# Kernel tuning notes

Measured on AMD Instinct MI355X. Metric: run time of the kernel, lower is better.

## Reference

```python
import jax, jax.numpy as jnp
import numpy as np

N = 16384          # input points
IN_PLANES = 64
OUT_PLANES = 128
STRIDE = 4
NSAMPLE = 16
M = N // STRIDE    # sampled points
EPS = 1e-5         # BatchNorm eps


def setup_inputs() -> dict:
    key = jax.random.key(0)
    k1, k2, k3 = jax.random.split(key, 3)
    p = jax.random.uniform(k1, (N, 3), dtype=jnp.float32) * 10.0   # xyz coords
    x = jax.random.normal(k2, (N, IN_PLANES), dtype=jnp.float32)
    o = jnp.array([N], dtype=jnp.int32)                            # single-batch offsets
    W = jax.random.normal(k3, (OUT_PLANES, 3 + IN_PLANES), dtype=jnp.float32) / np.sqrt(3 + IN_PLANES)
    gamma = jnp.ones((OUT_PLANES,), dtype=jnp.float32)
    beta = jnp.zeros((OUT_PLANES,), dtype=jnp.float32)
    return {"p": p, "x": x, "o": o, "W": W, "gamma": gamma, "beta": beta}


def _fps(p, m):
    """Furthest point sampling, starting from point 0 (matches pointops)."""
    n = p.shape[0]

    def step(carry, _):
        dist, last = carry
        d = jnp.sum((p - p[last]) ** 2, axis=1)       # (N,)
        dist = jnp.minimum(dist, d)
        nxt = jnp.argmax(dist).astype(jnp.int32)
        return (dist, nxt), nxt

    init = (jnp.full((n,), 1e10, dtype=jnp.float32), jnp.int32(0))
    _, idxs = jax.lax.scan(step, init, None, length=m - 1)
    return jnp.concatenate([jnp.zeros((1,), jnp.int32), idxs])


def _transition_down(p, x, W, gamma, beta):
    idx = _fps(p, M)
    n_p = p[idx]                                                    # (M,3)
    # kNN query: squared distances (M,N), take NSAMPLE nearest
    d2 = (jnp.sum(n_p ** 2, axis=1, keepdims=True)
          + jnp.sum(p ** 2, axis=1)[None, :]
          - 2.0 * n_p @ p.T)
    _, knn = jax.lax.top_k(-d2, NSAMPLE)                            # (M,NSAMPLE)
    rel = p[knn] - n_p[:, None, :]                                  # grouped relative xyz (M,S,3)
    feats = jnp.concatenate([rel, x[knn]], axis=-1)                 # (M,S,3+C) use_xyz=True
    y = jnp.einsum('msc,oc->mso', feats, W)                         # linear, no bias (M,S,O)
    # BatchNorm1d (training mode): normalize over batch (M) and length (S) dims
    mean = jnp.mean(y, axis=(0, 1))
    var = jnp.var(y, axis=(0, 1))
    y = (y - mean) * jax.lax.rsqrt(var + EPS) * gamma + beta
    y = jax.nn.relu(y)
    y = jnp.max(y, axis=1)                                          # MaxPool1d over nsample -> (M,O)
    return n_p, y


def reference(p, x, o, W, gamma, beta):
    n_p, y = _transition_down(p, x, W, gamma, beta)
    n_o = (o // STRIDE).astype(jnp.int32)
    return (n_p, y, n_o)
```

## Files before the change

### kernel.cpp

```cpp
#include <hip/hip_runtime.h>

#define N_PTS   16384
#define M_PTS   4096
#define NS      16
#define C_IN    64
#define C_FEAT  67
#define C_OUT   128
#define QPB     8
#define GEMM_BLOCKS (M_PTS / QPB)
#define N_O_POS (M_PTS*3 + M_PTS*C_OUT)

__global__ __launch_bounds__(1024)
void fps_kernel(const float* __restrict__ p, int* __restrict__ fidx)
{
#pragma clang fp contract(off)
    const int t    = threadIdx.x;
    const int lane = t & 63;
    const int wid  = t >> 6;

    float px[16], py[16], pz[16], dist[16];
#pragma unroll
    for (int k = 0; k < 16; ++k) {
        const int i = t + (k << 10);
        px[k] = p[3*i+0]; py[k] = p[3*i+1]; pz[k] = p[3*i+2];
        dist[k] = 1e10f;
    }

    __shared__ float swv[16];
    __shared__ int   swi[16];
    __shared__ float sq[4];

    if (t == 0) fidx[0] = 0;
    float qx = p[0], qy = p[1], qz = p[2];

    for (int it = 1; it < M_PTS; ++it) {
        float bv = -1.0f; int bi = 0x7fffffff;
#pragma unroll
        for (int k = 0; k < 16; ++k) {
            const float dx = px[k] - qx;
            const float dy = py[k] - qy;
            const float dz = pz[k] - qz;
            float d = dx*dx + dy*dy;
            d = d + dz*dz;
            const float nd = fminf(dist[k], d);
            dist[k] = nd;
            const bool take = nd > bv;
            bv = take ? nd : bv;
            bi = take ? (t + (k << 10)) : bi;
        }
#pragma unroll
        for (int off = 1; off < 64; off <<= 1) {
            const float ov = __shfl_xor(bv, off, 64);
            const int   oi = __shfl_xor(bi, off, 64);
            const bool take = (ov > bv) || (ov == bv && oi < bi);
            bv = take ? ov : bv;  bi = take ? oi : bi;
        }
        if (lane == 0) { swv[wid] = bv; swi[wid] = bi; }
        __syncthreads();
        float v2 = swv[lane & 15]; int i2 = swi[lane & 15];
#pragma unroll
        for (int off = 1; off < 16; off <<= 1) {
            const float ov = __shfl_xor(v2, off, 64);
            const int   oi = __shfl_xor(i2, off, 64);
            const bool take = (ov > v2) || (ov == v2 && oi < i2);
            v2 = take ? ov : v2;  i2 = take ? oi : i2;
        }
        const int cur = i2;
        if (t == (cur & 1023)) {
            const int k = cur >> 10;
            float ax = 0.f, ay = 0.f, az = 0.f;
#pragma unroll
            for (int k2 = 0; k2 < 16; ++k2) {
                if (k2 == k) { ax = px[k2]; ay = py[k2]; az = pz[k2]; }
            }
            sq[0] = ax; sq[1] = ay; sq[2] = az;
            fidx[it] = cur;
        }
        __syncthreads();
        qx = sq[0]; qy = sq[1]; qz = sq[2];
    }
}

__global__ __launch_bounds__(256)
void knn_kernel(const float* __restrict__ p, const int* __restrict__ fidx,
                int* __restrict__ knn_out, float* __restrict__ out_np)
{
    const int lane = threadIdx.x & 63;
    const int wid  = threadIdx.x >> 6;
    const int m    = blockIdx.x * 4 + wid;

    const int iq = fidx[m];
    const float qx = p[3*iq+0], qy = p[3*iq+1], qz = p[3*iq+2];
    if (lane == 0) { out_np[m*3+0] = qx; out_np[m*3+1] = qy; out_np[m*3+2] = qz; }

    float d16[16]; int i16[16];
#pragma unroll
    for (int jj = 0; jj < 16; ++jj) {
        const int j = jj*64 + lane;
        const float dx = p[3*j+0]-qx, dy = p[3*j+1]-qy, dz = p[3*j+2]-qz;
        d16[jj] = fmaf(dx, dx, fmaf(dy, dy, dz*dz));
        i16[jj] = j;
    }
    float wv = d16[0];
#pragma unroll
    for (int k = 1; k < 16; ++k) wv = fmaxf(wv, d16[k]);

    for (int jj = 16; jj < 256; ++jj) {
        const int j = jj*64 + lane;
        const float dx = p[3*j+0]-qx, dy = p[3*j+1]-qy, dz = p[3*j+2]-qz;
        const float d = fmaf(dx, dx, fmaf(dy, dy, dz*dz));
        if (d < wv) {
            bool done = false;
#pragma unroll
            for (int k = 0; k < 16; ++k) {
                const bool is = (!done) && (d16[k] == wv);
                d16[k] = is ? d : d16[k];
                i16[k] = is ? j : i16[k];
                done = done || is;
            }
            wv = d16[0];
#pragma unroll
            for (int k = 1; k < 16; ++k) wv = fmaxf(wv, d16[k]);
        }
    }

    float lmv; int lmi;
    {
        lmv = d16[0]; lmi = i16[0];
#pragma unroll
        for (int k = 1; k < 16; ++k) {
            const bool tk = (d16[k] < lmv) || (d16[k] == lmv && i16[k] < lmi);
            lmv = tk ? d16[k] : lmv;  lmi = tk ? i16[k] : lmi;
        }
    }
    int mykn = 0;
    for (int r = 0; r < 16; ++r) {
        float v = lmv; int ii = lmi;
#pragma unroll
        for (int off = 1; off < 64; off <<= 1) {
            const float ov = __shfl_xor(v, off, 64);
            const int   oi = __shfl_xor(ii, off, 64);
            const bool tk = (ov < v) || (ov == v && oi < ii);
            v = tk ? ov : v;  ii = tk ? oi : ii;
        }
        if (lane == r) mykn = ii;
        if (lmi == ii) {
#pragma unroll
            for (int k = 0; k < 16; ++k)
                d16[k] = (i16[k] == ii) ? 3.4e38f : d16[k];
            lmv = d16[0]; lmi = i16[0];
#pragma unroll
            for (int k = 1; k < 16; ++k) {
                const bool tk = (d16[k] < lmv) || (d16[k] == lmv && i16[k] < lmi);
                lmv = tk ? d16[k] : lmv;  lmi = tk ? i16[k] : lmi;
            }
        }
    }
    if (lane < 16) knn_out[m*16 + lane] = mykn;
}

template <int PHASE>
__global__ __launch_bounds__(256)
void gemm_kernel(const float* __restrict__ p, const float* __restrict__ x,
                 const int* __restrict__ knn, const float* __restrict__ W,
                 const float* __restrict__ np_buf, float* __restrict__ part,
                 const float* __restrict__ scsh, float* __restrict__ out_y)
{
    __shared__ float w_lds[C_OUT * C_FEAT];
    __shared__ float feats[NS * 68];
    __shared__ float tmp[512];

    const int tid = threadIdx.x;
    for (int e = tid; e < C_OUT * C_FEAT; e += 256) w_lds[e] = W[e];
    __syncthreads();

    const int o  = tid & 127;
    const int s0 = (tid >> 7) * 8;
    float wreg[C_FEAT];
#pragma unroll
    for (int c = 0; c < C_FEAT; ++c) wreg[c] = w_lds[o * C_FEAT + c];

    float sc = 0.f, sh = 0.f;
    if (PHASE == 1) { sc = scsh[o]; sh = scsh[128 + o]; }

    float lsum = 0.f, lsq = 0.f;

    for (int ml = 0; ml < QPB; ++ml) {
        const int m = blockIdx.x * QPB + ml;
        __syncthreads();
        for (int e = tid; e < NS * C_FEAT; e += 256) {
            const int s = e / C_FEAT;
            const int c = e - s * C_FEAT;
            const int j = knn[m * NS + s];
            float v;
            if (c < 3) v = p[3*j + c] - np_buf[m*3 + c];
            else       v = x[j * C_IN + (c - 3)];
            feats[s * 68 + c] = v;
        }
        __syncthreads();

        float mx = 0.0f;
#pragma unroll
        for (int s8 = 0; s8 < 8; ++s8) {
            const int s = s0 + s8;
            const float4* fr = (const float4*)&feats[s * 68];
            float a = 0.f;
#pragma unroll
            for (int c4 = 0; c4 < 16; ++c4) {
                const float4 f = fr[c4];
                a = fmaf(f.x, wreg[c4*4+0], a);
                a = fmaf(f.y, wreg[c4*4+1], a);
                a = fmaf(f.z, wreg[c4*4+2], a);
                a = fmaf(f.w, wreg[c4*4+3], a);
            }
            a = fmaf(feats[s*68+64], wreg[64], a);
            a = fmaf(feats[s*68+65], wreg[65], a);
            a = fmaf(feats[s*68+66], wreg[66], a);
            if (PHASE == 0) { lsum += a; lsq = fmaf(a, a, lsq); }
            else {
                float v = fmaf(a, sc, sh);
                v = fmaxf(v, 0.f);
                mx = fmaxf(mx, v);
            }
        }
        if (PHASE == 1) {
            tmp[tid] = mx;
            __syncthreads();
            if (tid < 128) out_y[m * C_OUT + o] = fmaxf(tmp[tid], tmp[tid + 128]);
        }
    }

    if (PHASE == 0) {
        tmp[tid] = lsum; tmp[256 + tid] = lsq;
        __syncthreads();
        if (tid < 128) {
            part[blockIdx.x * 256 + o]       = tmp[tid] + tmp[tid + 128];
            part[blockIdx.x * 256 + 128 + o] = tmp[256 + tid] + tmp[256 + tid + 128];
        }
    }
}

__global__ __launch_bounds__(128)
void stats_kernel(const float* __restrict__ part, const float* __restrict__ gamma,
                  const float* __restrict__ beta, float* __restrict__ scsh,
                  float* __restrict__ out)
{
    const int o = threadIdx.x;
    float s = 0.f, s2 = 0.f;
    for (int b = 0; b < GEMM_BLOCKS; ++b) {
        s  += part[b * 256 + o];
        s2 += part[b * 256 + 128 + o];
    }
    const float inv  = 1.0f / 65536.0f;
    const float mean = s * inv;
    const float var  = fmaf(s2, inv, -mean * mean);
    const float sc   = gamma[o] * rsqrtf(var + 1e-5f);
    const float sh   = fmaf(-mean, sc, beta[o]);
    scsh[o] = sc; scsh[128 + o] = sh;
    if (o == 0) out[N_O_POS] = 4096.0f;
}

extern "C" void kernel_launch(void* const* d_in, const int* in_sizes, int n_in,
                              void* d_out, int out_size, void* d_ws, size_t ws_size,
                              hipStream_t stream)
{
    const float* p     = (const float*)d_in[0];
    const float* x     = (const float*)d_in[1];
    const float* W     = (const float*)d_in[3];
    const float* gamma = (const float*)d_in[4];
    const float* beta  = (const float*)d_in[5];
    float* out = (float*)d_out;

    int*   fidx = (int*)d_ws;
    int*   knn  = fidx + M_PTS;
    float* part = (float*)(knn + M_PTS * NS);
    float* scsh = part + GEMM_BLOCKS * 256;

    float* out_np = out;
    float* out_y  = out + M_PTS * 3;

    fps_kernel<<<dim3(1), dim3(1024), 0, stream>>>(p, fidx);
    knn_kernel<<<dim3(M_PTS / 4), dim3(256), 0, stream>>>(p, fidx, knn, out_np);
    gemm_kernel<0><<<dim3(GEMM_BLOCKS), dim3(256), 0, stream>>>(
        p, x, knn, W, out_np, part, scsh, out_y);
    stats_kernel<<<dim3(1), dim3(128), 0, stream>>>(part, gamma, beta, scsh, out);
    gemm_kernel<1><<<dim3(GEMM_BLOCKS), dim3(256), 0, stream>>>(
        p, x, knn, W, out_np, part, scsh, out_y);
}
```

Before: 10.16 ms.

## Morton-sort points and skip FPS distance updates via per-thread bounding boxes

```diff
diff --git a/kernel.cpp b/kernel.cpp
--- a/kernel.cpp
+++ b/kernel.cpp
@@ -10,74 +10,152 @@
 #define GEMM_BLOCKS (M_PTS / QPB)
 #define N_O_POS (M_PTS*3 + M_PTS*C_OUT)
 
+#define FPS_T   512
+#define PPT     32
+
+__device__ __forceinline__ unsigned spread3(unsigned x)
+{
+    x = (x | (x << 16)) & 0x030000FFu;
+    x = (x | (x << 8))  & 0x0300F00Fu;
+    x = (x | (x << 4))  & 0x030C30C3u;
+    x = (x | (x << 2))  & 0x09249249u;
+    return x;
+}
+
 __global__ __launch_bounds__(1024)
-void fps_kernel(const float* __restrict__ p, int* __restrict__ fidx)
+void morton_sort_kernel(const float* __restrict__ p, unsigned* __restrict__ keys)
+{
+    __shared__ unsigned k_lds[N_PTS];
+    const int t = threadIdx.x;
+#pragma unroll
+    for (int s = 0; s < 16; ++s) {
+        const int i = t + (s << 10);
+        const float xx = p[3*i+0], yy = p[3*i+1], zz = p[3*i+2];
+        unsigned cx = (unsigned)fminf(fmaxf(xx * 6.4f, 0.f), 63.f);
+        unsigned cy = (unsigned)fminf(fmaxf(yy * 6.4f, 0.f), 63.f);
+        unsigned cz = (unsigned)fminf(fmaxf(zz * 6.4f, 0.f), 63.f);
+        const unsigned code = spread3(cx) | (spread3(cy) << 1) | (spread3(cz) << 2);
+        k_lds[i] = (code << 14) | (unsigned)i;
+    }
+    __syncthreads();
+    for (unsigned kk = 2; kk <= (unsigned)N_PTS; kk <<= 1) {
+        for (unsigned jj = kk >> 1; jj >= 1; jj >>= 1) {
+            for (int s = 0; s < 16; ++s) {
+                const int i = t + (s << 10);
+                const int ixj = i ^ (int)jj;
+                if (ixj > i) {
+                    const unsigned a = k_lds[i], b = k_lds[ixj];
+                    const bool up = ((i & kk) == 0);
+                    if (up ? (a > b) : (a < b)) { k_lds[i] = b; k_lds[ixj] = a; }
+                }
+            }
+            __syncthreads();
+        }
+    }
+#pragma unroll
+    for (int s = 0; s < 16; ++s) {
+        const int i = t + (s << 10);
+        keys[i] = k_lds[i];
+    }
+}
+
+__global__ __launch_bounds__(FPS_T)
+void fps_kernel(const float* __restrict__ p, const unsigned* __restrict__ keys,
+                int* __restrict__ fidx)
 {
 #pragma clang fp contract(off)
     const int t    = threadIdx.x;
     const int lane = t & 63;
     const int wid  = t >> 6;
 
-    float px[16], py[16], pz[16], dist[16];
-#pragma unroll
-    for (int k = 0; k < 16; ++k) {
-        const int i = t + (k << 10);
-        px[k] = p[3*i+0]; py[k] = p[3*i+1]; pz[k] = p[3*i+2];
+    float px[PPT], py[PPT], pz[PPT], dist[PPT];
+    int   oi[PPT];
+    float lox =  3e38f, loy =  3e38f, loz =  3e38f;
+    float hix = -3e38f, hiy = -3e38f, hiz = -3e38f;
+
+#pragma unroll
+    for (int k = 0; k < PPT; ++k) {
+        const unsigned key = keys[t * PPT + k];
+        const int j = (int)(key & 16383u);
+        oi[k] = j;
+        px[k] = p[3*j+0]; py[k] = p[3*j+1]; pz[k] = p[3*j+2];
         dist[k] = 1e10f;
-    }
-
-    __shared__ float swv[16];
-    __shared__ int   swi[16];
-    __shared__ float sq[4];
+        lox = fminf(lox, px[k]); hix = fmaxf(hix, px[k]);
+        loy = fminf(loy, py[k]); hiy = fmaxf(hiy, py[k]);
+        loz = fminf(loz, pz[k]); hiz = fmaxf(hiz, pz[k]);
+    }
+
+    __shared__ float  swv[8];
+    __shared__ int    swi[8];
+    __shared__ float4 sqv;
 
     if (t == 0) fidx[0] = 0;
-    float qx = p[0], qy = p[1], qz = p[2];
+#pragma unroll
+    for (int k = 0; k < PPT; ++k)
+        if (oi[k] == 0) sqv = make_float4(px[k], py[k], pz[k], 0.f);
+
+    float mymax = 1e10f;  int myidx = -1;
+    float bx = 0.f, by = 0.f, bz = 0.f;
+    int lastwin = 0;
+
+    __syncthreads();
 
     for (int it = 1; it < M_PTS; ++it) {
-        float bv = -1.0f; int bi = 0x7fffffff;
-#pragma unroll
-        for (int k = 0; k < 16; ++k) {
-            const float dx = px[k] - qx;
-            const float dy = py[k] - qy;
-            const float dz = pz[k] - qz;
-            float d = dx*dx + dy*dy;
-            d = d + dz*dz;
-            const float nd = fminf(dist[k], d);
-            dist[k] = nd;
-            const bool take = nd > bv;
-            bv = take ? nd : bv;
-            bi = take ? (t + (k << 10)) : bi;
-        }
-#pragma unroll
-        for (int off = 1; off < 64; off <<= 1) {
-            const float ov = __shfl_xor(bv, off, 64);
-            const int   oi = __shfl_xor(bi, off, 64);
-            const bool take = (ov > bv) || (ov == bv && oi < bi);
-            bv = take ? ov : bv;  bi = take ? oi : bi;
-        }
-        if (lane == 0) { swv[wid] = bv; swi[wid] = bi; }
-        __syncthreads();
-        float v2 = swv[lane & 15]; int i2 = swi[lane & 15];
-#pragma unroll
-        for (int off = 1; off < 16; off <<= 1) {
+        const float4 q4 = sqv;
+        const float qx = q4.x, qy = q4.y, qz = q4.z;
+
+        const float gx = fmaxf(fmaxf(lox - qx, qx - hix), 0.f);
+        const float gy = fmaxf(fmaxf(loy - qy, qy - hiy), 0.f);
+        const float gz = fmaxf(fmaxf(loz - qz, qz - hiz), 0.f);
+        const float dlow = (gx*gx + gy*gy + gz*gz) * 0.99999f;
+
+        const bool doflush = (dlow < mymax) || (myidx == lastwin);
+        if (doflush) {
+            float bv = -1.f; int bi = 0x7fffffff;
+            float cx = 0.f, cy = 0.f, cz = 0.f;
+#pragma unroll
+            for (int k = 0; k < PPT; ++k) {
+                const float dx = px[k] - qx;
+                const float dy = py[k] - qy;
+                const float dz = pz[k] - qz;
+                float d = dx*dx + dy*dy;
+                d = d + dz*dz;
+                const float nd = fminf(dist[k], d);
+                dist[k] = nd;
+                const bool tk = (nd > bv) || (nd == bv && oi[k] < bi);
+                bv = tk ? nd : bv;  bi = tk ? oi[k] : bi;
+                cx = tk ? px[k] : cx; cy = tk ? py[k] : cy; cz = tk ? pz[k] : cz;
+            }
+            mymax = bv; myidx = bi; bx = cx; by = cy; bz = cz;
+        }
+        const unsigned long long ch = __ballot(doflush);
+        if (ch) {
+            float v = mymax; int ii = myidx;
+#pragma unroll
+            for (int off = 1; off < 64; off <<= 1) {
+                const float ov = __shfl_xor(v, off, 64);
+                const int   oo = __shfl_xor(ii, off, 64);
+                const bool tk = (ov > v) || (ov == v && oo < ii);
+                v = tk ? ov : v;  ii = tk ? oo : ii;
+            }
+            if (lane == 0) { swv[wid] = v; swi[wid] = ii; }
+        }
+        __syncthreads();
+
+        float v2 = swv[lane & 7];  int i2 = swi[lane & 7];
+#pragma unroll
+        for (int off = 1; off < 8; off <<= 1) {
             const float ov = __shfl_xor(v2, off, 64);
-            const int   oi = __shfl_xor(i2, off, 64);
-            const bool take = (ov > v2) || (ov == v2 && oi < i2);
-            v2 = take ? ov : v2;  i2 = take ? oi : i2;
-        }
-        const int cur = i2;
-        if (t == (cur & 1023)) {
-            const int k = cur >> 10;
-            float ax = 0.f, ay = 0.f, az = 0.f;
-#pragma unroll
-            for (int k2 = 0; k2 < 16; ++k2) {
-                if (k2 == k) { ax = px[k2]; ay = py[k2]; az = pz[k2]; }
-            }
-            sq[0] = ax; sq[1] = ay; sq[2] = az;
-            fidx[it] = cur;
-        }
-        __syncthreads();
-        qx = sq[0]; qy = sq[1]; qz = sq[2];
+            const int   oo = __shfl_xor(i2, off, 64);
+            const bool tk = (ov > v2) || (ov == v2 && oo < i2);
+            v2 = tk ? ov : v2;  i2 = tk ? oo : i2;
+        }
+        lastwin = i2;
+        if (myidx == i2) {
+            sqv = make_float4(bx, by, bz, 0.f);
+            fidx[it] = i2;
+        }
+        __syncthreads();
     }
 }
 
@@ -139,9 +217,9 @@
 #pragma unroll
         for (int off = 1; off < 64; off <<= 1) {
             const float ov = __shfl_xor(v, off, 64);
-            const int   oi = __shfl_xor(ii, off, 64);
-            const bool tk = (ov < v) || (ov == v && oi < ii);
-            v = tk ? ov : v;  ii = tk ? oi : ii;
+            const int   oo = __shfl_xor(ii, off, 64);
+            const bool tk = (ov < v) || (ov == v && oo < ii);
+            v = tk ? ov : v;  ii = tk ? oo : ii;
         }
         if (lane == r) mykn = ii;
         if (lmi == ii) {
@@ -271,15 +349,17 @@
     const float* beta  = (const float*)d_in[5];
     float* out = (float*)d_out;
 
-    int*   fidx = (int*)d_ws;
-    int*   knn  = fidx + M_PTS;
-    float* part = (float*)(knn + M_PTS * NS);
-    float* scsh = part + GEMM_BLOCKS * 256;
+    int*      fidx = (int*)d_ws;
+    int*      knn  = fidx + M_PTS;
+    float*    part = (float*)(knn + M_PTS * NS);
+    float*    scsh = part + GEMM_BLOCKS * 256;
+    unsigned* keys = (unsigned*)(scsh + 256);
 
     float* out_np = out;
     float* out_y  = out + M_PTS * 3;
 
-    fps_kernel<<<dim3(1), dim3(1024), 0, stream>>>(p, fidx);
+    morton_sort_kernel<<<dim3(1), dim3(1024), 0, stream>>>(p, keys);
+    fps_kernel<<<dim3(1), dim3(FPS_T), 0, stream>>>(p, keys, fidx);
     knn_kernel<<<dim3(M_PTS / 4), dim3(256), 0, stream>>>(p, fidx, knn, out_np);
     gemm_kernel<0><<<dim3(GEMM_BLOCKS), dim3(256), 0, stream>>>(
         p, x, knn, W, out_np, part, scsh, out_y);
```

Measured after the change: 14.45 ms. 1.42x slower.
